# Kernel tuning notes

Hardware: AMD Instinct MI355X
Metric: run time of the kernel (lower is better)

The kernel has to match this reference:

```python
import jax, jax.numpy as jnp
import numpy as np

N = 50000
E = 800000
D_IN = 384
D_H = 128
D_MLP = 128
K = 16


def layer_norm(x, g, b, eps=1e-5):
    m = x.mean(-1, keepdims=True)
    v = ((x - m) ** 2).mean(-1, keepdims=True)
    return (x - m) / jnp.sqrt(v + eps) * g + b


def setup_inputs() -> dict:
    key = jax.random.key(0)
    ks = jax.random.split(key, 16)
    s = lambda d: 1.0 / np.sqrt(d)
    return {
        "x": jax.random.normal(ks[0], (N, D_IN), jnp.float32),
        "edge_index": jax.random.randint(ks[1], (2, E), 0, N, jnp.int64),
        # GCNConv 1
        "W1": jax.random.normal(ks[2], (D_IN, D_H), jnp.float32) * s(D_IN),
        "b1": jnp.zeros((D_H,), jnp.float32),
        "g1": jnp.ones((D_H,), jnp.float32),
        "be1": jnp.zeros((D_H,), jnp.float32),
        # GCNConv 2
        "W2": jax.random.normal(ks[3], (D_H, D_H), jnp.float32) * s(D_H),
        "b2": jnp.zeros((D_H,), jnp.float32),
        "g2": jnp.ones((D_H,), jnp.float32),
        "be2": jnp.zeros((D_H,), jnp.float32),
        # residual projection (input_dim != conv_hidden)
        "rW": jax.random.normal(ks[4], (D_IN, D_H), jnp.float32) * s(D_IN),
        "rb": jnp.zeros((D_H,), jnp.float32),
        "rg": jnp.ones((D_H,), jnp.float32),
        "rbe": jnp.zeros((D_H,), jnp.float32),
        # MLP head
        "mW1": jax.random.normal(ks[5], (D_H, D_MLP), jnp.float32) * s(D_H),
        "mb1": jnp.zeros((D_MLP,), jnp.float32),
        "mg": jnp.ones((D_MLP,), jnp.float32),
        "mbe": jnp.zeros((D_MLP,), jnp.float32),
        "mW2": jax.random.normal(ks[6], (D_MLP, K), jnp.float32) * s(D_MLP),
        "mb2": jnp.zeros((K,), jnp.float32),
    }


def reference(x, edge_index, W1, b1, g1, be1, W2, b2, g2, be2,
              rW, rb, rg, rbe, mW1, mb1, mg, mbe, mW2, mb2):
    n = x.shape[0]
    loops = jnp.arange(n, dtype=edge_index.dtype)
    src = jnp.concatenate([edge_index[0], loops])  # [E+N]
    dst = jnp.concatenate([edge_index[1], loops])
    # symmetric GCN normalization with self-loops
    deg = jax.ops.segment_sum(jnp.ones_like(src, x.dtype), dst, num_segments=n)
    dinv = jnp.where(deg > 0, jax.lax.rsqrt(deg), 0.0)
    norm = dinv[src] * dinv[dst]  # [E+N]

    def gcn_conv(h, W, b):
        hw = h @ W  # [N, D_H]
        msg = hw[src] * norm[:, None]  # gather + scale, [E+N, D_H]
        return jax.ops.segment_sum(msg, dst, num_segments=n) + b

    # layer 1 with projected residual
    h = jax.nn.elu(layer_norm(gcn_conv(x, W1, b1), g1, be1))
    h = h + layer_norm(x @ rW + rb, rg, rbe)
    # layer 2 with identity residual
    h = jax.nn.elu(layer_norm(gcn_conv(h, W2, b2), g2, be2)) + h
    # MLP head (dropout inactive in eval) + softmax over clusters
    z = jax.nn.elu(layer_norm(h @ mW1 + mb1, mg, mbe))
    H = z @ mW2 + mb2
    return jax.nn.softmax(H, axis=1)
```

## Files before the change

kernel.cpp:

```cpp
#include <hip/hip_runtime.h>

#define DH 128

typedef __attribute__((ext_vector_type(8))) short short8;
typedef __attribute__((ext_vector_type(4))) float f32x4;

__device__ __forceinline__ float wave_sum(float v) {
    #pragma unroll
    for (int o = 32; o > 0; o >>= 1) v += __shfl_xor(v, o, 64);
    return v;
}

__device__ __forceinline__ void ln_pair(float v0, float v1, float& o0, float& o1) {
    float m = wave_sum(v0 + v1) * (1.f / 128.f);
    float d0 = v0 - m, d1 = v1 - m;
    float var = wave_sum(d0 * d0 + d1 * d1) * (1.f / 128.f);
    float inv = rsqrtf(var + 1e-5f);
    o0 = d0 * inv; o1 = d1 * inv;
}

__device__ __forceinline__ float elu(float x) { return x > 0.f ? x : expm1f(x); }

__device__ __forceinline__ unsigned short f2bf(float f) {
    unsigned u = __float_as_uint(f);
    u += 0x7fffu + ((u >> 16) & 1u);
    return (unsigned short)(u >> 16);
}
__device__ __forceinline__ float bfl(unsigned u) { return __uint_as_float(u << 16); }
__device__ __forceinline__ float bfh(unsigned u) { return __uint_as_float(u & 0xffff0000u); }
__device__ __forceinline__ unsigned pack_bf2(float a, float b) {
    return (unsigned)f2bf(a) | ((unsigned)f2bf(b) << 16);
}
__device__ __forceinline__ short8 cvt8(float4 v0, float4 v1) {
    short8 o;
    o[0] = (short)f2bf(v0.x); o[1] = (short)f2bf(v0.y);
    o[2] = (short)f2bf(v0.z); o[3] = (short)f2bf(v0.w);
    o[4] = (short)f2bf(v1.x); o[5] = (short)f2bf(v1.y);
    o[6] = (short)f2bf(v1.z); o[7] = (short)f2bf(v1.w);
    return o;
}

__global__ __launch_bounds__(256) void conv_x_k(const float* __restrict__ x,
                                                unsigned short* __restrict__ xb,
                                                long long n8)
{
    long long i = (long long)blockIdx.x * 256 + threadIdx.x;
    long long stride = (long long)gridDim.x * 256;
    for (; i < n8; i += stride) {
        float4 v0 = *(const float4*)(x + i * 8);
        float4 v1 = *(const float4*)(x + i * 8 + 4);
        *(short8*)(xb + i * 8) = cvt8(v0, v1);
    }
}

__global__ void zero_int_k(int* __restrict__ p, int n) {
    int i = blockIdx.x * 256 + threadIdx.x;
    if (i < n) p[i] = 0;
}

__global__ void deg_count_k(const int* __restrict__ dst, int* __restrict__ deg, int E) {
    int e = blockIdx.x * 256 + threadIdx.x;
    if (e < E) atomicAdd(&deg[dst[e]], 1);
}

__global__ __launch_bounds__(1024) void scan_part_k(const int* __restrict__ deg,
                                                    int* __restrict__ rowptr,
                                                    int* __restrict__ bsum,
                                                    float* __restrict__ dinv, int n)
{
    __shared__ int wsum[16];
    const int tid = threadIdx.x, lane = tid & 63, wid = tid >> 6;
    int i = blockIdx.x * 1024 + tid;
    int v = (i < n) ? deg[i] : 0;
    if (i < n) dinv[i] = rsqrtf((float)(v + 1));
    int s = v;
    #pragma unroll
    for (int o = 1; o < 64; o <<= 1) {
        int t = __shfl_up(s, o, 64);
        if (lane >= o) s += t;
    }
    if (lane == 63) wsum[wid] = s;
    __syncthreads();
    if (tid < 16) {
        int ws = wsum[tid];
        #pragma unroll
        for (int o = 1; o < 16; o <<= 1) {
            int t = __shfl_up(ws, o, 64);
            if (tid >= o) ws += t;
        }
        wsum[tid] = ws;
    }
    __syncthreads();
    int excl = (wid ? wsum[wid - 1] : 0) + s - v;
    if (i < n) rowptr[i] = excl;
    if (tid == 0) bsum[blockIdx.x] = wsum[15];
}

__global__ void scan_top_k(int* __restrict__ bsum, int* __restrict__ rowptr_n, int nb) {
    int lane = threadIdx.x;
    int carry = 0;
    for (int base = 0; base < nb; base += 64) {
        int i = base + lane;
        int v = (i < nb) ? bsum[i] : 0;
        int s = v;
        #pragma unroll
        for (int o = 1; o < 64; o <<= 1) {
            int t = __shfl_up(s, o, 64);
            if (lane >= o) s += t;
        }
        if (i < nb) bsum[i] = carry + s - v;
        carry += __shfl(s, 63, 64);
    }
    if (lane == 0) *rowptr_n = carry;
}

__global__ void scan_add_k(const int* __restrict__ bsum, int* __restrict__ rowptr,
                           int* __restrict__ cursor, int n)
{
    int i = blockIdx.x * 256 + threadIdx.x;
    if (i < n) {
        int v = rowptr[i] + bsum[i >> 10];
        rowptr[i] = v;
        cursor[i] = v;
    }
}

__global__ void fill_k(const int* __restrict__ src, const int* __restrict__ dst,
                       const float* __restrict__ dinv, int* __restrict__ cursor,
                       int2* __restrict__ csr, int E)
{
    int e = blockIdx.x * 256 + threadIdx.x;
    if (e < E) {
        int s = src[e], d = dst[e];
        float w = dinv[s] * dinv[d];
        int p = atomicAdd(&cursor[d], 1);
        csr[p] = make_int2(s, __float_as_int(w));
    }
}

__global__ void repack_all_k(const float* __restrict__ W1, const float* __restrict__ rW,
                             const float* __restrict__ W2, const float* __restrict__ mW1,
                             unsigned short* __restrict__ Wp)
{
    int idx = blockIdx.x * 256 + threadIdx.x;
    if (idx >= 131072) return;
    const float* W; int base;
    if (idx < 49152)       { W = W1;  base = 0; }
    else if (idx < 98304)  { W = rW;  base = 49152; }
    else if (idx < 114688) { W = W2;  base = 98304; }
    else                   { W = mW1; base = 114688; }
    int l = idx - base;
    int kb = l >> 12, rem = l & 4095;
    int nn = rem >> 5, ki = rem & 31;
    Wp[idx] = f2bf(W[(kb * 32 + ki) * DH + nn]);
}

template<int K, int NMAT>
__global__ __launch_bounds__(256, 3) void mfma_gemm(
    const unsigned short* __restrict__ A,
    const unsigned short* __restrict__ Bp1, const float* __restrict__ ba,
    const unsigned short* __restrict__ Bp2, const float* __restrict__ bb,
    unsigned short* __restrict__ outa, unsigned short* __restrict__ outb, int n)
{
    constexpr int NKB = K / 32;
    constexpr int SB   = NKB * 64 * 32;
    constexpr int SEP  = 128 * 72;
    constexpr int SMEM = SB > SEP ? SB : SEP;
    __shared__ __align__(16) unsigned short smem[SMEM];

    const int tid = threadIdx.x;
    const int wid = tid >> 6, lane = tid & 63;
    const int m16 = lane & 15, q = lane >> 4;
    const int mat = (NMAT == 2) ? (int)(blockIdx.y >> 1) : 0;
    const int c0  = (blockIdx.y & 1) * 64;
    const unsigned short* Bp = mat ? Bp2 : Bp1;
    unsigned short* outp = mat ? outb : outa;
    const float* bias = mat ? bb : ba;
    const long long rowbase = (long long)blockIdx.x * 128;

    long long r0 = rowbase + wid * 32 + m16;       if (r0 > (long long)n - 1) r0 = n - 1;
    long long r1 = rowbase + wid * 32 + 16 + m16;  if (r1 > (long long)n - 1) r1 = n - 1;

    f32x4 acc[2][4];
    const f32x4 zero = {0.f, 0.f, 0.f, 0.f};
    #pragma unroll
    for (int mi = 0; mi < 2; ++mi)
        #pragma unroll
        for (int nj = 0; nj < 4; ++nj) acc[mi][nj] = zero;

    short8 ha[3][2];
    short8 bf[2][4];

    auto fetchA = [&](int kb, int buf) {
        ha[buf][0] = *(const short8*)(A + r0 * K + kb * 32 + q * 8);
        ha[buf][1] = *(const short8*)(A + r1 * K + kb * 32 + q * 8);
    };
    auto fetchB = [&](int kb, int buf) {
        #pragma unroll
        for (int nj = 0; nj < 4; ++nj)
            bf[buf][nj] = *(const short8*)(smem + kb * 2048 + (nj * 16 + m16) * 32 + q * 8);
    };

    fetchA(0, 0);
    if constexpr (NKB > 1) fetchA(1, 1);

    #pragma unroll
    for (int t = tid; t < K * 8; t += 256) {
        int k8 = t & 3, cl = (t >> 2) & 63, kb = t >> 8;
        *(short8*)(smem + kb * 2048 + cl * 32 + k8 * 8) =
            *(const short8*)(Bp + (long long)kb * 4096 + (c0 + cl) * 32 + k8 * 8);
    }
    __syncthreads();

    fetchB(0, 0);
    #pragma unroll
    for (int kb = 0; kb < NKB; ++kb) {
        if (kb + 2 < NKB) fetchA(kb + 2, (kb + 2) % 3);
        if (kb + 1 < NKB) fetchB(kb + 1, (kb + 1) & 1);
        const int ca = kb % 3, cb = kb & 1;
        #pragma unroll
        for (int mi = 0; mi < 2; ++mi)
            #pragma unroll
            for (int nj = 0; nj < 4; ++nj)
                acc[mi][nj] = __builtin_amdgcn_mfma_f32_16x16x32_bf16(ha[ca][mi], bf[cb][nj], acc[mi][nj], 0, 0, 0);
    }

    __syncthreads();
    #pragma unroll
    for (int nj = 0; nj < 4; ++nj) {
        int cl = nj * 16 + m16;
        float bv = bias ? bias[c0 + cl] : 0.f;
        #pragma unroll
        for (int mi = 0; mi < 2; ++mi)
            #pragma unroll
            for (int r = 0; r < 4; ++r)
                smem[(wid * 32 + mi * 16 + q * 4 + r) * 72 + cl] = f2bf(acc[mi][nj][r] + bv);
    }
    __syncthreads();
    #pragma unroll
    for (int h = 0; h < 4; ++h) {
        int idx = tid + h * 256;
        int row = idx >> 3, c8 = idx & 7;
        long long grow = rowbase + row;
        if (grow < n)
            *(short8*)(outp + grow * DH + c0 + c8 * 8) = *(const short8*)(smem + row * 72 + c8 * 8);
    }
}

__device__ __forceinline__ void gather_row(
    const unsigned* __restrict__ hw, const int2* __restrict__ csr,
    int beg, int end, int lane, float& o0, float& o1)
{
    float s0[4] = {0.f, 0.f, 0.f, 0.f};
    float s1[4] = {0.f, 0.f, 0.f, 0.f};
    int p = beg;
    for (; p + 15 < end; p += 16) {
        int2 e[16];
        #pragma unroll
        for (int j = 0; j < 16; ++j) e[j] = csr[p + j];
        unsigned u[16];
        #pragma unroll
        for (int j = 0; j < 16; ++j) u[j] = hw[(long long)e[j].x * 64 + lane];
        #pragma unroll
        for (int j = 0; j < 16; ++j) {
            float w = __int_as_float(e[j].y);
            s0[j & 3] = fmaf(w, bfl(u[j]), s0[j & 3]);
            s1[j & 3] = fmaf(w, bfh(u[j]), s1[j & 3]);
        }
    }
    for (; p + 7 < end; p += 8) {
        int2 e[8];
        #pragma unroll
        for (int j = 0; j < 8; ++j) e[j] = csr[p + j];
        unsigned u[8];
        #pragma unroll
        for (int j = 0; j < 8; ++j) u[j] = hw[(long long)e[j].x * 64 + lane];
        #pragma unroll
        for (int j = 0; j < 8; ++j) {
            float w = __int_as_float(e[j].y);
            s0[j & 3] = fmaf(w, bfl(u[j]), s0[j & 3]);
            s1[j & 3] = fmaf(w, bfh(u[j]), s1[j & 3]);
        }
    }
    for (; p + 3 < end; p += 4) {
        int2 e[4];
        #pragma unroll
        for (int j = 0; j < 4; ++j) e[j] = csr[p + j];
        unsigned u[4];
        #pragma unroll
        for (int j = 0; j < 4; ++j) u[j] = hw[(long long)e[j].x * 64 + lane];
        #pragma unroll
        for (int j = 0; j < 4; ++j) {
            float w = __int_as_float(e[j].y);
            s0[j] = fmaf(w, bfl(u[j]), s0[j]);
            s1[j] = fmaf(w, bfh(u[j]), s1[j]);
        }
    }
    for (; p < end; ++p) {
        int2 e0 = csr[p];
        unsigned u0 = hw[(long long)e0.x * 64 + lane];
        float w = __int_as_float(e0.y);
        s0[0] = fmaf(w, bfl(u0), s0[0]);
        s1[0] = fmaf(w, bfh(u0), s1[0]);
    }
    o0 = (s0[0] + s0[1]) + (s0[2] + s0[3]);
    o1 = (s1[0] + s1[1]) + (s1[2] + s1[3]);
}

__global__ __launch_bounds__(256) void gfuse1_k(
    const unsigned* __restrict__ hw, const unsigned* __restrict__ proj,
    const int* __restrict__ rowptr, const int2* __restrict__ csr,
    const float* __restrict__ dinv,
    const float* __restrict__ b1, const float* __restrict__ g1, const float* __restrict__ be1,
    const float* __restrict__ rg, const float* __restrict__ rbe,
    unsigned* __restrict__ hout, int n)
{
    int row = blockIdx.x * 4 + (threadIdx.x >> 6);
    if (row >= n) return;
    int lane = threadIdx.x & 63;
    float a0, a1;
    gather_row(hw, csr, rowptr[row], rowptr[row + 1], lane, a0, a1);
    long long off = (long long)row * 64;
    float di = dinv[row], sl = di * di;
    unsigned us = hw[off + lane];
    float2 bv  = *(const float2*)(b1 + 2 * lane);
    float2 gv  = *(const float2*)(g1 + 2 * lane);
    float2 bev = *(const float2*)(be1 + 2 * lane);
    float2 rgv = *(const float2*)(rg + 2 * lane);
    float2 rbv = *(const float2*)(rbe + 2 * lane);
    float v0 = a0 + sl * bfl(us) + bv.x;
    float v1 = a1 + sl * bfh(us) + bv.y;
    float o0, o1; ln_pair(v0, v1, o0, o1);
    float t0 = elu(o0 * gv.x + bev.x);
    float t1 = elu(o1 * gv.y + bev.y);
    unsigned up = proj[off + lane];
    float q0, q1; ln_pair(bfl(up), bfh(up), q0, q1);
    hout[off + lane] = pack_bf2(t0 + q0 * rgv.x + rbv.x, t1 + q1 * rgv.y + rbv.y);
}

__global__ __launch_bounds__(256) void gfuse2_k(
    const unsigned* __restrict__ hw, const unsigned* __restrict__ hprev,
    const int* __restrict__ rowptr, const int2* __restrict__ csr,
    const float* __restrict__ dinv,
    const float* __restrict__ b2, const float* __restrict__ g2, const float* __restrict__ be2,
    unsigned* __restrict__ h2, int n)
{
    int row = blockIdx.x * 4 + (threadIdx.x >> 6);
    if (row >= n) return;
    int lane = threadIdx.x & 63;
    float a0, a1;
    gather_row(hw, csr, rowptr[row], rowptr[row + 1], lane, a0, a1);
    long long off = (long long)row * 64;
    float di = dinv[row], sl = di * di;
    unsigned us = hw[off + lane];
    float2 bv  = *(const float2*)(b2 + 2 * lane);
    float2 gv  = *(const float2*)(g2 + 2 * lane);
    float2 bev = *(const float2*)(be2 + 2 * lane);
    float v0 = a0 + sl * bfl(us) + bv.x;
    float v1 = a1 + sl * bfh(us) + bv.y;
    float o0, o1; ln_pair(v0, v1, o0, o1);
    float t0 = elu(o0 * gv.x + bev.x);
    float t1 = elu(o1 * gv.y + bev.y);
    unsigned uh = hprev[off + lane];
    h2[off + lane] = pack_bf2(t0 + bfl(uh), t1 + bfh(uh));
}

__global__ __launch_bounds__(256) void head_k(
    const unsigned* __restrict__ zraw, const float* __restrict__ g, const float* __restrict__ be,
    const float* __restrict__ mW2, const float* __restrict__ mb2,
    float* __restrict__ out, int n)
{
    int row = blockIdx.x * 4 + (threadIdx.x >> 6);
    if (row >= n) return;
    int lane = threadIdx.x & 63;
    unsigned u = zraw[(long long)row * 64 + lane];
    float o0, o1; ln_pair(bfl(u), bfh(u), o0, o1);
    float2 gv  = *(const float2*)(g + 2 * lane);
    float2 bev = *(const float2*)(be + 2 * lane);
    float z0 = elu(o0 * gv.x + bev.x);
    float z1 = elu(o1 * gv.y + bev.y);
    int k = lane & 15, seg = lane >> 4;
    float acc = 0.f;
    #pragma unroll
    for (int t = 0; t < 16; ++t) {
        int srcl = seg * 16 + t;
        float zz0 = __shfl(z0, srcl, 64);
        float zz1 = __shfl(z1, srcl, 64);
        int c = seg * 32 + 2 * t;
        acc = fmaf(zz0, mW2[c * 16 + k], acc);
        acc = fmaf(zz1, mW2[(c + 1) * 16 + k], acc);
    }
    acc += __shfl_xor(acc, 32, 64);
    acc += __shfl_xor(acc, 16, 64);
    float hk = acc + mb2[k];
    float mx = hk;
    #pragma unroll
    for (int o = 8; o > 0; o >>= 1) mx = fmaxf(mx, __shfl_xor(mx, o, 64));
    float e = expf(hk - mx);
    float s = e;
    #pragma unroll
    for (int o = 8; o > 0; o >>= 1) s += __shfl_xor(s, o, 64);
    if (lane < 16) out[(long long)row * 16 + k] = e / s;
}

static inline size_t align16(size_t x) { return (x + 15) & ~(size_t)15; }

extern "C" void kernel_launch(void* const* d_in, const int* in_sizes, int n_in,
                              void* d_out, int out_size, void* d_ws, size_t ws_size,
                              hipStream_t stream)
{
    const float* x   = (const float*)d_in[0];
    const int*   ei  = (const int*)d_in[1];
    const float* W1  = (const float*)d_in[2];
    const float* b1  = (const float*)d_in[3];
    const float* g1  = (const float*)d_in[4];
    const float* be1 = (const float*)d_in[5];
    const float* W2  = (const float*)d_in[6];
    const float* b2  = (const float*)d_in[7];
    const float* g2  = (const float*)d_in[8];
    const float* be2 = (const float*)d_in[9];
    const float* rW  = (const float*)d_in[10];
    const float* rb  = (const float*)d_in[11];
    const float* rg  = (const float*)d_in[12];
    const float* rbe = (const float*)d_in[13];
    const float* mW1 = (const float*)d_in[14];
    const float* mb1 = (const float*)d_in[15];
    const float* mg  = (const float*)d_in[16];
    const float* mbe = (const float*)d_in[17];
    const float* mW2 = (const float*)d_in[18];
    const float* mb2 = (const float*)d_in[19];
    float* out = (float*)d_out;

    const int n = in_sizes[0] / 384;
    const int E = in_sizes[1] / 2;
    const int* src = ei;
    const int* dst = ei + E;

    char* w = (char*)d_ws;
    int* deg     = (int*)w;   w += align16((size_t)n * 4);
    int* rowptr  = (int*)w;   w += align16((size_t)(n + 1) * 4);
    int* cursor  = (int*)w;   w += align16((size_t)n * 4);
    float* dinv  = (float*)w; w += align16((size_t)n * 4);
    int* bsum    = (int*)w;   w += align16((size_t)1024 * 4);
    int2* csr    = (int2*)w;  w += align16((size_t)E * 8);
    unsigned short* xb   = (unsigned short*)w; w += align16((size_t)n * 384 * 2);
    unsigned short* hw1  = (unsigned short*)w; w += align16((size_t)n * DH * 2);
    unsigned short* proj = (unsigned short*)w; w += align16((size_t)n * DH * 2);
    unsigned short* hbuf = (unsigned short*)w; w += align16((size_t)n * DH * 2);
    unsigned short* Wp   = (unsigned short*)w; w += align16((size_t)131072 * 2);
    unsigned short* Wp1 = Wp;
    unsigned short* Wpr = Wp + 49152;
    unsigned short* Wp2 = Wp + 98304;
    unsigned short* WpM = Wp + 114688;
    unsigned short* hw2  = hw1;
    unsigned short* h2   = proj;
    unsigned short* zraw = hbuf;

    int gE = (E + 255) / 256;
    int gN = (n + 255) / 256;
    int nb = (n + 1023) / 1024;
    dim3 gGd((n + 127) / 128, 4);
    dim3 gGs((n + 127) / 128, 2);
    int gRow4 = (n + 3) / 4;

    conv_x_k<<<2048, 256, 0, stream>>>(x, xb, (long long)n * 48);
    repack_all_k<<<512, 256, 0, stream>>>(W1, rW, W2, mW1, Wp);

    zero_int_k<<<gN, 256, 0, stream>>>(deg, n);
    deg_count_k<<<gE, 256, 0, stream>>>(dst, deg, E);
    scan_part_k<<<nb, 1024, 0, stream>>>(deg, rowptr, bsum, dinv, n);
    scan_top_k<<<1, 64, 0, stream>>>(bsum, rowptr + n, nb);
    scan_add_k<<<gN, 256, 0, stream>>>(bsum, rowptr, cursor, n);
    fill_k<<<gE, 256, 0, stream>>>(src, dst, dinv, cursor, csr, E);

    mfma_gemm<384, 2><<<gGd, 256, 0, stream>>>(xb, Wp1, nullptr, Wpr, rb, hw1, proj, n);
    gfuse1_k<<<gRow4, 256, 0, stream>>>((unsigned*)hw1, (unsigned*)proj, rowptr, csr, dinv,
                                        b1, g1, be1, rg, rbe, (unsigned*)hbuf, n);

    mfma_gemm<128, 1><<<gGs, 256, 0, stream>>>(hbuf, Wp2, nullptr, nullptr, nullptr, hw2, nullptr, n);
    gfuse2_k<<<gRow4, 256, 0, stream>>>((unsigned*)hw2, (unsigned*)hbuf, rowptr, csr, dinv,
                                        b2, g2, be2, (unsigned*)h2, n);

    mfma_gemm<128, 1><<<gGs, 256, 0, stream>>>(h2, WpM, mb1, nullptr, nullptr, zraw, nullptr, n);
    head_k<<<gRow4, 256, 0, stream>>>((unsigned*)zraw, mg, mbe, mW2, mb2, out, n);
}
```

Measured before the change: 435.3 us.

## Fuse MLP GEMM with head, split edge gather across half-waves, fold deg zeroing

The MLP first-layer GEMM is fused with the LayerNorm/ELU/projection/softmax head, so the intermediate z tensor no longer makes a round trip through global memory and one launch disappears. The GCN gather now has each half-wave take alternate edges and load 8-byte chunks (4 channels per lane), then combines the halves with a shuffle. The aim is more edges in flight per wave and wider loads, at the cost of duplicated LayerNorm work and a half-idle store. The zeroing of the degree array is folded into the x conversion kernel, removing another launch.

Result: slower. 487.1 us (+11.9%).

```diff
diff --git a/kernel.cpp b/kernel.cpp
--- a/kernel.cpp
+++ b/kernel.cpp
@@ -9,6 +9,14 @@
     #pragma unroll
     for (int o = 32; o > 0; o >>= 1) v += __shfl_xor(v, o, 64);
     return v;
+}
+
+__device__ __forceinline__ void ln_quad(float4 v, float4& o) {
+    float m = wave_sum(v.x + v.y + v.z + v.w) * (1.f / 256.f);
+    float dx = v.x - m, dy = v.y - m, dz = v.z - m, dw = v.w - m;
+    float var = wave_sum(dx * dx + dy * dy + dz * dz + dw * dw) * (1.f / 256.f);
+    float inv = rsqrtf(var + 1e-5f);
+    o = make_float4(dx * inv, dy * inv, dz * inv, dw * inv);
 }
 
 __device__ __forceinline__ void ln_pair(float v0, float v1, float& o0, float& o1) {
@@ -42,20 +50,16 @@
 
 __global__ __launch_bounds__(256) void conv_x_k(const float* __restrict__ x,
                                                 unsigned short* __restrict__ xb,
-                                                long long n8)
+                                                long long n8, int* __restrict__ deg, int n)
 {
     long long i = (long long)blockIdx.x * 256 + threadIdx.x;
+    if (i < n) deg[i] = 0;
     long long stride = (long long)gridDim.x * 256;
     for (; i < n8; i += stride) {
         float4 v0 = *(const float4*)(x + i * 8);
         float4 v1 = *(const float4*)(x + i * 8 + 4);
         *(short8*)(xb + i * 8) = cvt8(v0, v1);
     }
-}
-
-__global__ void zero_int_k(int* __restrict__ p, int n) {
-    int i = blockIdx.x * 256 + threadIdx.x;
-    if (i < n) p[i] = 0;
 }
 
 __global__ void deg_count_k(const int* __restrict__ dst, int* __restrict__ deg, int E) {
@@ -247,64 +251,160 @@
     }
 }
 
-__device__ __forceinline__ void gather_row(
+__global__ __launch_bounds__(256, 3) void gemm_head_k(
+    const unsigned short* __restrict__ A, const unsigned short* __restrict__ Bp,
+    const float* __restrict__ mb1,
+    const float* __restrict__ g, const float* __restrict__ be,
+    const float* __restrict__ mW2, const float* __restrict__ mb2,
+    float* __restrict__ out, int n)
+{
+    __shared__ __align__(16) unsigned short smem[16384];
+    const int tid = threadIdx.x;
+    const int wid = tid >> 6, lane = tid & 63;
+    const int m16 = lane & 15, q = lane >> 4;
+    const int rh = wid >> 1, ch = wid & 1;
+    const long long rowbase = (long long)blockIdx.x * 64;
+
+    long long r0 = rowbase + rh * 32 + m16;       if (r0 > (long long)n - 1) r0 = n - 1;
+    long long r1 = rowbase + rh * 32 + 16 + m16;  if (r1 > (long long)n - 1) r1 = n - 1;
+
+    f32x4 acc[2][4];
+    const f32x4 zero = {0.f, 0.f, 0.f, 0.f};
+    #pragma unroll
+    for (int mi = 0; mi < 2; ++mi)
+        #pragma unroll
+        for (int nj = 0; nj < 4; ++nj) acc[mi][nj] = zero;
+
+    short8 ha[3][2];
+    short8 bf[2][4];
+
+    auto fetchA = [&](int kb, int buf) {
+        ha[buf][0] = *(const short8*)(A + r0 * 128 + kb * 32 + q * 8);
+        ha[buf][1] = *(const short8*)(A + r1 * 128 + kb * 32 + q * 8);
+    };
+    auto fetchB = [&](int kb, int buf) {
+        #pragma unroll
+        for (int nj = 0; nj < 4; ++nj)
+            bf[buf][nj] = *(const short8*)(smem + kb * 4096 + (ch * 64 + nj * 16 + m16) * 32 + q * 8);
+    };
+
+    fetchA(0, 0);
+    fetchA(1, 1);
+    #pragma unroll
+    for (int t = tid; t < 2048; t += 256)
+        *(short8*)(smem + t * 8) = *(const short8*)(Bp + t * 8);
+    __syncthreads();
+
+    fetchB(0, 0);
+    #pragma unroll
+    for (int kb = 0; kb < 4; ++kb) {
+        if (kb + 2 < 4) fetchA(kb + 2, (kb + 2) % 3);
+        if (kb + 1 < 4) fetchB(kb + 1, (kb + 1) & 1);
+        const int ca = kb % 3, cb = kb & 1;
+        #pragma unroll
+        for (int mi = 0; mi < 2; ++mi)
+            #pragma unroll
+            for (int nj = 0; nj < 4; ++nj)
+                acc[mi][nj] = __builtin_amdgcn_mfma_f32_16x16x32_bf16(ha[ca][mi], bf[cb][nj], acc[mi][nj], 0, 0, 0);
+    }
+
+    __syncthreads();
+    #pragma unroll
+    for (int nj = 0; nj < 4; ++nj) {
+        int cl = ch * 64 + nj * 16 + m16;
+        float bv = mb1[cl];
+        #pragma unroll
+        for (int mi = 0; mi < 2; ++mi)
+            #pragma unroll
+            for (int r = 0; r < 4; ++r)
+                smem[(rh * 32 + mi * 16 + q * 4 + r) * 136 + cl] = f2bf(acc[mi][nj][r] + bv);
+    }
+    __syncthreads();
+
+    const unsigned* zl = (const unsigned*)smem;
+    int k = lane & 15, seg = lane >> 4;
+    float2 gv  = *(const float2*)(g + 2 * lane);
+    float2 bev = *(const float2*)(be + 2 * lane);
+    for (int rr = 0; rr < 16; ++rr) {
+        int lrow = wid * 16 + rr;
+        long long grow = rowbase + lrow;
+        if (grow >= n) break;
+        unsigned u = zl[lrow * 68 + lane];
+        float o0, o1; ln_pair(bfl(u), bfh(u), o0, o1);
+        float z0 = elu(o0 * gv.x + bev.x);
+        float z1 = elu(o1 * gv.y + bev.y);
+        float acch = 0.f;
+        #pragma unroll
+        for (int t = 0; t < 16; ++t) {
+            int srcl = seg * 16 + t;
+            float zz0 = __shfl(z0, srcl, 64);
+            float zz1 = __shfl(z1, srcl, 64);
+            int c = seg * 32 + 2 * t;
+            acch = fmaf(zz0, mW2[c * 16 + k], acch);
+            acch = fmaf(zz1, mW2[(c + 1) * 16 + k], acch);
+        }
+        acch += __shfl_xor(acch, 32, 64);
+        acch += __shfl_xor(acch, 16, 64);
+        float hk = acch + mb2[k];
+        float mx = hk;
+        #pragma unroll
+        for (int o = 8; o > 0; o >>= 1) mx = fmaxf(mx, __shfl_xor(mx, o, 64));
+        float e = expf(hk - mx);
+        float s = e;
+        #pragma unroll
+        for (int o = 8; o > 0; o >>= 1) s += __shfl_xor(s, o, 64);
+        if (lane < 16) out[grow * 16 + k] = e / s;
+    }
+}
+
+__device__ __forceinline__ void gather_row2(
     const unsigned* __restrict__ hw, const int2* __restrict__ csr,
-    int beg, int end, int lane, float& o0, float& o1)
-{
-    float s0[4] = {0.f, 0.f, 0.f, 0.f};
-    float s1[4] = {0.f, 0.f, 0.f, 0.f};
+    int beg, int end, int half, int c2, float4& o)
+{
+    float s0 = 0.f, s1 = 0.f, s2 = 0.f, s3 = 0.f;
     int p = beg;
     for (; p + 15 < end; p += 16) {
-        int2 e[16];
-        #pragma unroll
-        for (int j = 0; j < 16; ++j) e[j] = csr[p + j];
-        unsigned u[16];
-        #pragma unroll
-        for (int j = 0; j < 16; ++j) u[j] = hw[(long long)e[j].x * 64 + lane];
-        #pragma unroll
-        for (int j = 0; j < 16; ++j) {
-            float w = __int_as_float(e[j].y);
-            s0[j & 3] = fmaf(w, bfl(u[j]), s0[j & 3]);
-            s1[j & 3] = fmaf(w, bfh(u[j]), s1[j & 3]);
+        uint2 u[8]; float w[8];
+        #pragma unroll
+        for (int j = 0; j < 8; ++j) {
+            int2 e0 = csr[p + 2 * j];
+            int2 e1 = csr[p + 2 * j + 1];
+            int srcn = half ? e1.x : e0.x;
+            w[j] = __int_as_float(half ? e1.y : e0.y);
+            u[j] = *(const uint2*)(hw + (long long)srcn * 64 + c2 * 2);
         }
-    }
-    for (; p + 7 < end; p += 8) {
-        int2 e[8];
-        #pragma unroll
-        for (int j = 0; j < 8; ++j) e[j] = csr[p + j];
-        unsigned u[8];
-        #pragma unroll
-        for (int j = 0; j < 8; ++j) u[j] = hw[(long long)e[j].x * 64 + lane];
         #pragma unroll
         for (int j = 0; j < 8; ++j) {
-            float w = __int_as_float(e[j].y);
-            s0[j & 3] = fmaf(w, bfl(u[j]), s0[j & 3]);
-            s1[j & 3] = fmaf(w, bfh(u[j]), s1[j & 3]);
+            s0 = fmaf(w[j], bfl(u[j].x), s0);
+            s1 = fmaf(w[j], bfh(u[j].x), s1);
+            s2 = fmaf(w[j], bfl(u[j].y), s2);
+            s3 = fmaf(w[j], bfh(u[j].y), s3);
         }
     }
-    for (; p + 3 < end; p += 4) {
-        int2 e[4];
-        #pragma unroll
-        for (int j = 0; j < 4; ++j) e[j] = csr[p + j];
-        unsigned u[4];
-        #pragma unroll
-        for (int j = 0; j < 4; ++j) u[j] = hw[(long long)e[j].x * 64 + lane];
-        #pragma unroll
-        for (int j = 0; j < 4; ++j) {
-            float w = __int_as_float(e[j].y);
-            s0[j] = fmaf(w, bfl(u[j]), s0[j]);
-            s1[j] = fmaf(w, bfh(u[j]), s1[j]);
-        }
-    }
-    for (; p < end; ++p) {
+    for (; p + 1 < end; p += 2) {
+        int2 e0 = csr[p], e1 = csr[p + 1];
+        int srcn = half ? e1.x : e0.x;
+        float w = __int_as_float(half ? e1.y : e0.y);
+        uint2 u = *(const uint2*)(hw + (long long)srcn * 64 + c2 * 2);
+        s0 = fmaf(w, bfl(u.x), s0);
+        s1 = fmaf(w, bfh(u.x), s1);
+        s2 = fmaf(w, bfl(u.y), s2);
+        s3 = fmaf(w, bfh(u.y), s3);
+    }
+    if (p < end) {
         int2 e0 = csr[p];
-        unsigned u0 = hw[(long long)e0.x * 64 + lane];
-        float w = __int_as_float(e0.y);
-        s0[0] = fmaf(w, bfl(u0), s0[0]);
-        s1[0] = fmaf(w, bfh(u0), s1[0]);
-    }
-    o0 = (s0[0] + s0[1]) + (s0[2] + s0[3]);
-    o1 = (s1[0] + s1[1]) + (s1[2] + s1[3]);
+        float w = half ? 0.f : __int_as_float(e0.y);
+        uint2 u = *(const uint2*)(hw + (long long)e0.x * 64 + c2 * 2);
+        s0 = fmaf(w, bfl(u.x), s0);
+        s1 = fmaf(w, bfh(u.x), s1);
+        s2 = fmaf(w, bfl(u.y), s2);
+        s3 = fmaf(w, bfh(u.y), s3);
+    }
+    s0 += __shfl_xor(s0, 32, 64);
+    s1 += __shfl_xor(s1, 32, 64);
+    s2 += __shfl_xor(s2, 32, 64);
+    s3 += __shfl_xor(s3, 32, 64);
+    o = make_float4(s0, s1, s2, s3);
 }
 
 __global__ __launch_bounds__(256) void gfuse1_k(
@@ -318,24 +418,35 @@
     int row = blockIdx.x * 4 + (threadIdx.x >> 6);
     if (row >= n) return;
     int lane = threadIdx.x & 63;
-    float a0, a1;
-    gather_row(hw, csr, rowptr[row], rowptr[row + 1], lane, a0, a1);
+    int half = lane >> 5, c2 = lane & 31;
+    float4 a;
+    gather_row2(hw, csr, rowptr[row], rowptr[row + 1], half, c2, a);
     long long off = (long long)row * 64;
     float di = dinv[row], sl = di * di;
-    unsigned us = hw[off + lane];
-    float2 bv  = *(const float2*)(b1 + 2 * lane);
-    float2 gv  = *(const float2*)(g1 + 2 * lane);
-    float2 bev = *(const float2*)(be1 + 2 * lane);
-    float2 rgv = *(const float2*)(rg + 2 * lane);
-    float2 rbv = *(const float2*)(rbe + 2 * lane);
-    float v0 = a0 + sl * bfl(us) + bv.x;
-    float v1 = a1 + sl * bfh(us) + bv.y;
-    float o0, o1; ln_pair(v0, v1, o0, o1);
-    float t0 = elu(o0 * gv.x + bev.x);
-    float t1 = elu(o1 * gv.y + bev.y);
-    unsigned up = proj[off + lane];
-    float q0, q1; ln_pair(bfl(up), bfh(up), q0, q1);
-    hout[off + lane] = pack_bf2(t0 + q0 * rgv.x + rbv.x, t1 + q1 * rgv.y + rbv.y);
+    uint2 us = *(const uint2*)(hw + off + c2 * 2);
+    float4 bv  = *(const float4*)(b1 + 4 * c2);
+    float4 gv  = *(const float4*)(g1 + 4 * c2);
+    float4 bev = *(const float4*)(be1 + 4 * c2);
+    float4 rgv = *(const float4*)(rg + 4 * c2);
+    float4 rbv = *(const float4*)(rbe + 4 * c2);
+    float4 v = make_float4(a.x + sl * bfl(us.x) + bv.x,
+                           a.y + sl * bfh(us.x) + bv.y,
+                           a.z + sl * bfl(us.y) + bv.z,
+                           a.w + sl * bfh(us.y) + bv.w);
+    float4 o; ln_quad(v, o);
+    float t0 = elu(o.x * gv.x + bev.x);
+    float t1 = elu(o.y * gv.y + bev.y);
+    float t2 = elu(o.z * gv.z + bev.z);
+    float t3 = elu(o.w * gv.w + bev.w);
+    uint2 up = *(const uint2*)(proj + off + c2 * 2);
+    float4 pv = make_float4(bfl(up.x), bfh(up.x), bfl(up.y), bfh(up.y));
+    float4 qo; ln_quad(pv, qo);
+    if (!half) {
+        uint2 w2;
+        w2.x = pack_bf2(t0 + qo.x * rgv.x + rbv.x, t1 + qo.y * rgv.y + rbv.y);
+        w2.y = pack_bf2(t2 + qo.z * rgv.z + rbv.z, t3 + qo.w * rgv.w + rbv.w);
+        *(uint2*)(hout + off + c2 * 2) = w2;
+    }
 }
 
 __global__ __launch_bounds__(256) void gfuse2_k(
@@ -348,59 +459,31 @@
     int row = blockIdx.x * 4 + (threadIdx.x >> 6);
     if (row >= n) return;
     int lane = threadIdx.x & 63;
-    float a0, a1;
-    gather_row(hw, csr, rowptr[row], rowptr[row + 1], lane, a0, a1);
+    int half = lane >> 5, c2 = lane & 31;
+    float4 a;
+    gather_row2(hw, csr, rowptr[row], rowptr[row + 1], half, c2, a);
     long long off = (long long)row * 64;
     float di = dinv[row], sl = di * di;
-    unsigned us = hw[off + lane];
-    float2 bv  = *(const float2*)(b2 + 2 * lane);
-    float2 gv  = *(const float2*)(g2 + 2 * lane);
-    float2 bev = *(const float2*)(be2 + 2 * lane);
-    float v0 = a0 + sl * bfl(us) + bv.x;
-    float v1 = a1 + sl * bfh(us) + bv.y;
-    float o0, o1; ln_pair(v0, v1, o0, o1);
-    float t0 = elu(o0 * gv.x + bev.x);
-    float t1 = elu(o1 * gv.y + bev.y);
-    unsigned uh = hprev[off + lane];
-    h2[off + lane] = pack_bf2(t0 + bfl(uh), t1 + bfh(uh));
-}
-
-__global__ __launch_bounds__(256) void head_k(
-    const unsigned* __restrict__ zraw, const float* __restrict__ g, const float* __restrict__ be,
-    const float* __restrict__ mW2, const float* __restrict__ mb2,
-    float* __restrict__ out, int n)
-{
-    int row = blockIdx.x * 4 + (threadIdx.x >> 6);
-    if (row >= n) return;
-    int lane = threadIdx.x & 63;
-    unsigned u = zraw[(long long)row * 64 + lane];
-    float o0, o1; ln_pair(bfl(u), bfh(u), o0, o1);
-    float2 gv  = *(const float2*)(g + 2 * lane);
-    float2 bev = *(const float2*)(be + 2 * lane);
-    float z0 = elu(o0 * gv.x + bev.x);
-    float z1 = elu(o1 * gv.y + bev.y);
-    int k = lane & 15, seg = lane >> 4;
-    float acc = 0.f;
-    #pragma unroll
-    for (int t = 0; t < 16; ++t) {
-        int srcl = seg * 16 + t;
-        float zz0 = __shfl(z0, srcl, 64);
-        float zz1 = __shfl(z1, srcl, 64);
-        int c = seg * 32 + 2 * t;
-        acc = fmaf(zz0, mW2[c * 16 + k], acc);
-        acc = fmaf(zz1, mW2[(c + 1) * 16 + k], acc);
-    }
-    acc += __shfl_xor(acc, 32, 64);
-    acc += __shfl_xor(acc, 16, 64);
-    float hk = acc + mb2[k];
-    float mx = hk;
-    #pragma unroll
-    for (int o = 8; o > 0; o >>= 1) mx = fmaxf(mx, __shfl_xor(mx, o, 64));
-    float e = expf(hk - mx);
-    float s = e;
-    #pragma unroll
-    for (int o = 8; o > 0; o >>= 1) s += __shfl_xor(s, o, 64);
-    if (lane < 16) out[(long long)row * 16 + k] = e / s;
+    uint2 us = *(const uint2*)(hw + off + c2 * 2);
+    float4 bv  = *(const float4*)(b2 + 4 * c2);
+    float4 gv  = *(const float4*)(g2 + 4 * c2);
+    float4 bev = *(const float4*)(be2 + 4 * c2);
+    float4 v = make_float4(a.x + sl * bfl(us.x) + bv.x,
+                           a.y + sl * bfh(us.x) + bv.y,
+                           a.z + sl * bfl(us.y) + bv.z,
+                           a.w + sl * bfh(us.y) + bv.w);
+    float4 o; ln_quad(v, o);
+    float t0 = elu(o.x * gv.x + bev.x);
+    float t1 = elu(o.y * gv.y + bev.y);
+    float t2 = elu(o.z * gv.z + bev.z);
+    float t3 = elu(o.w * gv.w + bev.w);
+    if (!half) {
+        uint2 uh = *(const uint2*)(hprev + off + c2 * 2);
+        uint2 w2;
+        w2.x = pack_bf2(t0 + bfl(uh.x), t1 + bfh(uh.x));
+        w2.y = pack_bf2(t2 + bfl(uh.y), t3 + bfh(uh.y));
+        *(uint2*)(h2 + off + c2 * 2) = w2;
+    }
 }
 
 static inline size_t align16(size_t x) { return (x + 15) & ~(size_t)15; }
@@ -454,7 +537,6 @@
     unsigned short* WpM = Wp + 114688;
     unsigned short* hw2  = hw1;
     unsigned short* h2   = proj;
-    unsigned short* zraw = hbuf;
 
     int gE = (E + 255) / 256;
     int gN = (n + 255) / 256;
@@ -462,11 +544,11 @@
     dim3 gGd((n + 127) / 128, 4);
     dim3 gGs((n + 127) / 128, 2);
     int gRow4 = (n + 3) / 4;
-
-    conv_x_k<<<2048, 256, 0, stream>>>(x, xb, (long long)n * 48);
+    int gH = (n + 63) / 64;
+
+    conv_x_k<<<2048, 256, 0, stream>>>(x, xb, (long long)n * 48, deg, n);
     repack_all_k<<<512, 256, 0, stream>>>(W1, rW, W2, mW1, Wp);
 
-    zero_int_k<<<gN, 256, 0, stream>>>(deg, n);
     deg_count_k<<<gE, 256, 0, stream>>>(dst, deg, E);
     scan_part_k<<<nb, 1024, 0, stream>>>(deg, rowptr, bsum, dinv, n);
     scan_top_k<<<1, 64, 0, stream>>>(bsum, rowptr + n, nb);
@@ -481,6 +563,5 @@
     gfuse2_k<<<gRow4, 256, 0, stream>>>((unsigned*)hw2, (unsigned*)hbuf, rowptr, csr, dinv,
                                         b2, g2, be2, (unsigned*)h2, n);
 
-    mfma_gemm<128, 1><<<gGs, 256, 0, stream>>>(h2, WpM, mb1, nullptr, nullptr, zraw, nullptr, n);
-    head_k<<<gRow4, 256, 0, stream>>>((unsigned*)zraw, mg, mbe, mW2, mb2, out, n);
-}
+    gemm_head_k<<<gH, 256, 0, stream>>>(h2, WpM, mb1, mg, mbe, mW2, mb2, out, n);
+}
```
